# Kernel optimization log

Measured on AMD Instinct MI355X. Metric: run time of the kernel, lower is better.

Reference implementation:

```python
import jax, jax.numpy as jnp
import numpy as np

EPS = 1e-8
THRESHOLD_FACTOR = 0.5


def setup_inputs() -> dict:
    key = jax.random.key(0)
    k1, k2, k3 = jax.random.split(key, 3)
    B, S, D_IN, D_OUT = 4, 4096, 2048, 2048
    x = jax.random.normal(k1, (B, S, D_IN), dtype=jnp.float32)
    # kaiming-uniform-like init for weight
    bound = 1.0 / np.sqrt(D_IN)
    weight = jax.random.uniform(k2, (D_OUT, D_IN), dtype=jnp.float32,
                                minval=-np.sqrt(3.0) * bound, maxval=np.sqrt(3.0) * bound)
    row_scale = jnp.ones((D_OUT, 1), dtype=jnp.float32)
    bias = jax.random.uniform(k3, (D_OUT,), dtype=jnp.float32, minval=-bound, maxval=bound)
    g = jnp.ones((D_IN,), dtype=jnp.float32)  # input RMSNorm affine weight
    return {"x": x, "weight": weight, "row_scale": row_scale, "bias": bias, "g": g}


def _rms_norm(v, axis):
    return v * jax.lax.rsqrt(jnp.mean(v * v, axis=axis, keepdims=True) + EPS)


def reference(x, weight, row_scale, bias, g):
    # input RMSNorm with affine scale
    xn = _rms_norm(x, -1) * g  # [B,S,Din]
    # row RMSNorm of weight
    w = _rms_norm(weight, 1)  # [Dout,Din]
    # abs-mean threshold ternary quantization
    abs_mean = jnp.mean(jnp.abs(w), axis=1, keepdims=True)  # [Dout,1]
    mask = (jnp.abs(w) > THRESHOLD_FACTOR * abs_mean).astype(w.dtype)
    w_q = jnp.sign(w) * mask  # ternary {-1,0,1}
    # scaled dequant: per-row abs_mean and learned row_scale
    w_eff = w_q * abs_mean * row_scale  # [Dout,Din]
    out = jnp.einsum('bsd,od->bso', xn, w_eff) + bias
    return out
```

## Files before the change

kernel.cpp:

```cpp
#include <hip/hip_runtime.h>
#include <stdint.h>

#define EPSF 1e-8f

using i32x4 = __attribute__((ext_vector_type(4))) int;

__device__ __forceinline__ float wave_sum(float v) {
#pragma unroll
  for (int off = 32; off > 0; off >>= 1) v += __shfl_down(v, off, 64);
  return v;
}
__device__ __forceinline__ float wave_max(float v) {
#pragma unroll
  for (int off = 32; off > 0; off >>= 1) v = fmaxf(v, __shfl_down(v, off, 64));
  return v;
}

__global__ __launch_bounds__(256) void wquant_kernel(
    const float* __restrict__ w, const float* __restrict__ row_scale,
    signed char* __restrict__ wq, float* __restrict__ scale, int K) {
  const int row = blockIdx.x;
  const int t = threadIdx.x;
  const float* wr = w + (size_t)row * K;
  float4 v0 = reinterpret_cast<const float4*>(wr)[2 * t];
  float4 v1 = reinterpret_cast<const float4*>(wr)[2 * t + 1];
  float f[8] = {v0.x, v0.y, v0.z, v0.w, v1.x, v1.y, v1.z, v1.w};
  float sa = 0.f, sq = 0.f;
#pragma unroll
  for (int i = 0; i < 8; ++i) { sa += fabsf(f[i]); sq += f[i] * f[i]; }
  sa = wave_sum(sa);
  sq = wave_sum(sq);
  __shared__ float smA[4], smQ[4];
  const int wid = t >> 6;
  if ((t & 63) == 0) { smA[wid] = sa; smQ[wid] = sq; }
  __syncthreads();
  const float sumabs = smA[0] + smA[1] + smA[2] + smA[3];
  const float sumsq  = smQ[0] + smQ[1] + smQ[2] + smQ[3];
  const float absmean = sumabs / (float)K;
  const float thr = 0.5f * absmean;
  union { signed char c[8]; uint2 u; } pk;
#pragma unroll
  for (int i = 0; i < 8; ++i)
    pk.c[i] = (fabsf(f[i]) > thr) ? (f[i] > 0.f ? (signed char)1 : (signed char)-1)
                                  : (signed char)0;
  reinterpret_cast<uint2*>(wq + (size_t)row * K)[t] = pk.u;
  if (t == 0)
    scale[row] = absmean * rsqrtf(sumsq / (float)K + EPSF) * row_scale[row];
}

__global__ __launch_bounds__(256) void xnorm_kernel(
    const float* __restrict__ x, const float* __restrict__ g,
    signed char* __restrict__ xq, float* __restrict__ sx, int K) {
  const int row = blockIdx.x;
  const int t = threadIdx.x;
  const float* xr = x + (size_t)row * K;
  float4 v0 = reinterpret_cast<const float4*>(xr)[2 * t];
  float4 v1 = reinterpret_cast<const float4*>(xr)[2 * t + 1];
  float f[8] = {v0.x, v0.y, v0.z, v0.w, v1.x, v1.y, v1.z, v1.w};
  float sq = 0.f;
#pragma unroll
  for (int i = 0; i < 8; ++i) sq += f[i] * f[i];
  sq = wave_sum(sq);
  __shared__ float smQ[4], smM[4];
  const int wid = t >> 6;
  if ((t & 63) == 0) smQ[wid] = sq;
  __syncthreads();
  const float sumsq = smQ[0] + smQ[1] + smQ[2] + smQ[3];
  const float rs = rsqrtf(sumsq / (float)K + EPSF);
  float4 g0 = reinterpret_cast<const float4*>(g)[2 * t];
  float4 g1 = reinterpret_cast<const float4*>(g)[2 * t + 1];
  float gg[8] = {g0.x, g0.y, g0.z, g0.w, g1.x, g1.y, g1.z, g1.w};
  float vv[8]; float am = 0.f;
#pragma unroll
  for (int i = 0; i < 8; ++i) {
    vv[i] = f[i] * rs * gg[i];
    am = fmaxf(am, fabsf(vv[i]));
  }
  am = wave_max(am);
  if ((t & 63) == 0) smM[wid] = am;
  __syncthreads();
  const float amax = fmaxf(fmaxf(smM[0], smM[1]), fmaxf(smM[2], smM[3]));
  const float inv = amax > 0.f ? 127.f / amax : 0.f;
  union { signed char c[8]; uint2 u; } pk;
#pragma unroll
  for (int i = 0; i < 8; ++i)
    pk.c[i] = (signed char)__float2int_rn(vv[i] * inv);
  reinterpret_cast<uint2*>(xq + (size_t)row * K)[t] = pk.u;
  if (t == 0) sx[row] = amax > 0.f ? amax / 127.f : 0.f;
}


#define BAR() do { __builtin_amdgcn_sched_barrier(0); \
                   asm volatile("" ::: "memory"); \
                   __builtin_amdgcn_s_barrier(); \
                   asm volatile("" ::: "memory"); \
                   __builtin_amdgcn_sched_barrier(0); } while (0)
#define VM(n) asm volatile("s_waitcnt vmcnt(" #n ")" ::: "memory")

__global__ __launch_bounds__(512, 2) void gemm_kernel(
    const signed char* __restrict__ A,
    const signed char* __restrict__ B,
    const float* __restrict__ scale, const float* __restrict__ bias,
    const float* __restrict__ sx,
    float* __restrict__ C, int M, int N, int K) {
  __shared__ signed char lds[2][2][2][16384];

  const int tid  = threadIdx.x;
  const int lane = tid & 63;
  const int wid  = tid >> 6;
  const int wm   = wid >> 2;
  const int wn   = wid & 3;
  const int fr   = lane & 15;
  const int kq   = lane >> 4;

  const int nwg = gridDim.x;
  const int cpx = nwg >> 3;
  const int swz = (blockIdx.x & 7) * cpx + (blockIdx.x >> 3);
  const int NBN = N >> 8;
  const int bn = swz % NBN;
  const int bm = swz / NBN;
  const int mBase = bm * 256, nBase = bn * 256;

  const size_t Kb = (size_t)K;

  const int sr = tid >> 3;
  const int gsrc = ((tid & 7) - sr - (sr >> 3)) & 7;
  const char* Abyte = (const char*)A + (size_t)(mBase + sr) * Kb + gsrc * 16;
  const char* Bbyte = (const char*)B +
      (size_t)(nBase + ((sr >> 5) * 64) + (sr & 31)) * Kb + gsrc * 16;

#define STAGE_A(bufi, h, t) do { \
    __builtin_amdgcn_global_load_lds( \
      (const __attribute__((address_space(1))) void*)(Abyte + (size_t)((h) * 64) * Kb + (size_t)(t) * 128), \
      (__attribute__((address_space(3))) void*)(&lds[bufi][0][h][tid * 16]), 16, 0, 0); \
    __builtin_amdgcn_global_load_lds( \
      (const __attribute__((address_space(1))) void*)(Abyte + (size_t)(128 + (h) * 64) * Kb + (size_t)(t) * 128), \
      (__attribute__((address_space(3))) void*)(&lds[bufi][0][h][8192 + tid * 16]), 16, 0, 0); \
  } while (0)

#define STAGE_B(bufi, h, t) do { \
    __builtin_amdgcn_global_load_lds( \
      (const __attribute__((address_space(1))) void*)(Bbyte + (size_t)((h) * 32) * Kb + (size_t)(t) * 128), \
      (__attribute__((address_space(3))) void*)(&lds[bufi][1][h][tid * 16]), 16, 0, 0); \
    __builtin_amdgcn_global_load_lds( \
      (const __attribute__((address_space(1))) void*)(Bbyte + (size_t)(128 + (h) * 32) * Kb + (size_t)(t) * 128), \
      (__attribute__((address_space(3))) void*)(&lds[bufi][1][h][8192 + tid * 16]), 16, 0, 0); \
  } while (0)

  const int raBase = wm * 64 + fr;
  const int rbBase = wn * 32 + fr;
  const int pA = (raBase + (raBase >> 3)) & 7;
  const int pB = (rbBase + (rbBase >> 3)) & 7;

  i32x4 aF[4][2], bF[4][2];
  i32x4 acc[8][4];
#pragma unroll
  for (int m = 0; m < 8; ++m)
#pragma unroll
    for (int n = 0; n < 4; ++n) acc[m][n] = (i32x4){0, 0, 0, 0};

#define LDA(bufi, mg) do { \
    _Pragma("unroll") for (int mm = 0; mm < 4; ++mm) \
    _Pragma("unroll") for (int s = 0; s < 2; ++s) \
      aF[mm][s] = *(const i32x4*)&lds[bufi][0][mg][ \
          (raBase + mm * 16) * 128 + (((s * 4 + kq) + pA + 2 * mm) & 7) * 16]; \
  } while (0)

#define LDB(bufi, np) do { \
    _Pragma("unroll") for (int nn = 0; nn < 2; ++nn) \
    _Pragma("unroll") for (int s = 0; s < 2; ++s) \
      bF[(np) * 2 + nn][s] = *(const i32x4*)&lds[bufi][1][np][ \
          (rbBase + nn * 16) * 128 + (((s * 4 + kq) + pB + 2 * nn) & 7) * 16]; \
  } while (0)

#define MFMA_Q(mg, np) do { \
    __builtin_amdgcn_s_setprio(1); \
    _Pragma("unroll") for (int mm = 0; mm < 4; ++mm) \
    _Pragma("unroll") for (int nn = 0; nn < 2; ++nn) { \
      i32x4 c = acc[(mg) * 4 + mm][(np) * 2 + nn]; \
      c = __builtin_amdgcn_mfma_i32_16x16x64_i8(aF[mm][0], bF[(np) * 2 + nn][0], c, 0, 0, 0); \
      c = __builtin_amdgcn_mfma_i32_16x16x64_i8(aF[mm][1], bF[(np) * 2 + nn][1], c, 0, 0, 0); \
      acc[(mg) * 4 + mm][(np) * 2 + nn] = c; \
    } \
    __builtin_amdgcn_s_setprio(0); } while (0)

  const int crowBase = mBase + wm * 128 + kq * 4;
  const int ccolBase = nBase + wn * 64 + fr;

#define STORE_Q(mg, np) do { \
    float sxq_[4][4]; \
    _Pragma("unroll") for (int mm = 0; mm < 4; ++mm) \
    _Pragma("unroll") for (int r = 0; r < 4; ++r) \
      sxq_[mm][r] = sx[crowBase + ((mg) * 4 + mm) * 16 + r]; \
    _Pragma("unroll") for (int nn = 0; nn < 2; ++nn) { \
      const int gc = ccolBase + ((np) * 2 + nn) * 16; \
      const float sc = scale[gc]; \
      const float bi = bias[gc]; \
      _Pragma("unroll") for (int mm = 0; mm < 4; ++mm) { \
        const int r0 = crowBase + ((mg) * 4 + mm) * 16; \
        _Pragma("unroll") for (int r = 0; r < 4; ++r) \
          C[(size_t)(r0 + r) * (size_t)N + (size_t)gc] = \
              (float)acc[(mg) * 4 + mm][(np) * 2 + nn][r] * (sxq_[mm][r] * sc) + bi; \
      } } } while (0)

  STAGE_A(0, 0, 0); STAGE_B(0, 0, 0);
  STAGE_A(0, 1, 0); STAGE_B(0, 1, 0);
  STAGE_A(1, 0, 1); STAGE_B(1, 0, 1);
  VM(8);
  BAR();

  const int NT = K >> 7;
  for (int i = 0; i < (NT >> 1) - 1; ++i) {
    const int t1  = 2 * i + 1;
    const int tn0 = 2 * i + 2;
    const int tn1 = 2 * i + 3;
    LDA(0, 0); LDB(0, 0); STAGE_A(1, 1, t1); VM(6);
    BAR(); MFMA_Q(0, 0); BAR();
    LDB(0, 1); STAGE_B(1, 1, t1);
    BAR(); MFMA_Q(0, 1); BAR();
    LDA(0, 1); STAGE_A(0, 0, tn0);
    BAR(); MFMA_Q(1, 0); BAR();
    STAGE_B(0, 0, tn0); VM(8);
    BAR(); MFMA_Q(1, 1); BAR();
    LDA(1, 0); LDB(1, 0); STAGE_A(0, 1, tn0); VM(6);
    BAR(); MFMA_Q(0, 0); BAR();
    LDB(1, 1); STAGE_B(0, 1, tn0);
    BAR(); MFMA_Q(0, 1); BAR();
    LDA(1, 1); STAGE_A(1, 0, tn1);
    BAR(); MFMA_Q(1, 0); BAR();
    STAGE_B(1, 0, tn1); VM(8);
    BAR(); MFMA_Q(1, 1); BAR();
  }

  {
    const int tl = NT - 1;
    LDA(0, 0); LDB(0, 0); STAGE_A(1, 1, tl); VM(6);
    BAR(); MFMA_Q(0, 0); BAR();
    LDB(0, 1); STAGE_B(1, 1, tl);
    BAR(); MFMA_Q(0, 1); BAR();
    LDA(0, 1);
    BAR(); MFMA_Q(1, 0); BAR();
    VM(4);
    BAR(); MFMA_Q(1, 1); BAR();
    LDA(1, 0); LDB(1, 0); VM(0);
    BAR(); MFMA_Q(0, 0); STORE_Q(0, 0); BAR();
    LDB(1, 1);
    BAR(); MFMA_Q(0, 1); STORE_Q(0, 1); BAR();
    LDA(1, 1);
    BAR(); MFMA_Q(1, 0); STORE_Q(1, 0); BAR();
    MFMA_Q(1, 1); STORE_Q(1, 1);
  }
#undef STAGE_A
#undef STAGE_B
#undef LDA
#undef LDB
#undef MFMA_Q
#undef STORE_Q
}

extern "C" void kernel_launch(void* const* d_in, const int* in_sizes, int n_in,
                              void* d_out, int out_size, void* d_ws, size_t ws_size,
                              hipStream_t stream) {
  const float* x         = (const float*)d_in[0];
  const float* weight    = (const float*)d_in[1];
  const float* row_scale = (const float*)d_in[2];
  const float* bias      = (const float*)d_in[3];
  const float* g         = (const float*)d_in[4];
  float* out = (float*)d_out;

  const int Din  = in_sizes[4];
  const int Dout = in_sizes[3];
  const int Mrows = in_sizes[0] / Din;

  char* ws = (char*)d_ws;
  signed char* wq = (signed char*)ws;
  signed char* xq = (signed char*)(ws + (size_t)Dout * Din);
  float* scale = (float*)(ws + (size_t)Dout * Din + (size_t)Mrows * Din);
  float* sx = scale + Dout;

  wquant_kernel<<<Dout, 256, 0, stream>>>(weight, row_scale, wq, scale, Din);
  xnorm_kernel<<<Mrows, 256, 0, stream>>>(x, g, xq, sx, Din);
  const int grid = (Mrows / 256) * (Dout / 256);
  gemm_kernel<<<grid, 512, 0, stream>>>(xq, wq, scale, bias, sx, out,
                                        Mrows, Dout, Din);
}
```

Measured before the change: 124.4 us.

## Use XOR LDS swizzle and halve barriers in int8 MFMA GEMM main loop

```diff
diff --git a/kernel.cpp b/kernel.cpp
--- a/kernel.cpp
+++ b/kernel.cpp
@@ -124,7 +124,7 @@
   const size_t Kb = (size_t)K;
 
   const int sr = tid >> 3;
-  const int gsrc = ((tid & 7) - sr - (sr >> 3)) & 7;
+  const int gsrc = (tid & 7) ^ (sr & 7);
   const char* Abyte = (const char*)A + (size_t)(mBase + sr) * Kb + gsrc * 16;
   const char* Bbyte = (const char*)B +
       (size_t)(nBase + ((sr >> 5) * 64) + (sr & 31)) * Kb + gsrc * 16;
@@ -147,10 +147,9 @@
       (__attribute__((address_space(3))) void*)(&lds[bufi][1][h][8192 + tid * 16]), 16, 0, 0); \
   } while (0)
 
-  const int raBase = wm * 64 + fr;
-  const int rbBase = wn * 32 + fr;
-  const int pA = (raBase + (raBase >> 3)) & 7;
-  const int pB = (rbBase + (rbBase >> 3)) & 7;
+  const int slot0 = ((kq ^ (fr & 7)) << 4);
+  const int aRowB = (wm * 64 + fr) * 128;
+  const int bRowB = (wn * 32 + fr) * 128;
 
   i32x4 aF[4][2], bF[4][2];
   i32x4 acc[8][4];
@@ -163,14 +162,14 @@
     _Pragma("unroll") for (int mm = 0; mm < 4; ++mm) \
     _Pragma("unroll") for (int s = 0; s < 2; ++s) \
       aF[mm][s] = *(const i32x4*)&lds[bufi][0][mg][ \
-          (raBase + mm * 16) * 128 + (((s * 4 + kq) + pA + 2 * mm) & 7) * 16]; \
+          aRowB + mm * 2048 + (slot0 ^ (s << 6))]; \
   } while (0)
 
 #define LDB(bufi, np) do { \
     _Pragma("unroll") for (int nn = 0; nn < 2; ++nn) \
     _Pragma("unroll") for (int s = 0; s < 2; ++s) \
       bF[(np) * 2 + nn][s] = *(const i32x4*)&lds[bufi][1][np][ \
-          (rbBase + nn * 16) * 128 + (((s * 4 + kq) + pB + 2 * nn) & 7) * 16]; \
+          bRowB + nn * 2048 + (slot0 ^ (s << 6))]; \
   } while (0)
 
 #define MFMA_Q(mg, np) do { \
@@ -215,40 +214,40 @@
     const int tn0 = 2 * i + 2;
     const int tn1 = 2 * i + 3;
     LDA(0, 0); LDB(0, 0); STAGE_A(1, 1, t1); VM(6);
-    BAR(); MFMA_Q(0, 0); BAR();
+    BAR(); MFMA_Q(0, 0);
     LDB(0, 1); STAGE_B(1, 1, t1);
-    BAR(); MFMA_Q(0, 1); BAR();
+    BAR(); MFMA_Q(0, 1);
     LDA(0, 1); STAGE_A(0, 0, tn0);
-    BAR(); MFMA_Q(1, 0); BAR();
+    BAR(); MFMA_Q(1, 0);
     STAGE_B(0, 0, tn0); VM(8);
-    BAR(); MFMA_Q(1, 1); BAR();
+    BAR(); MFMA_Q(1, 1);
     LDA(1, 0); LDB(1, 0); STAGE_A(0, 1, tn0); VM(6);
-    BAR(); MFMA_Q(0, 0); BAR();
+    BAR(); MFMA_Q(0, 0);
     LDB(1, 1); STAGE_B(0, 1, tn0);
-    BAR(); MFMA_Q(0, 1); BAR();
+    BAR(); MFMA_Q(0, 1);
     LDA(1, 1); STAGE_A(1, 0, tn1);
-    BAR(); MFMA_Q(1, 0); BAR();
+    BAR(); MFMA_Q(1, 0);
     STAGE_B(1, 0, tn1); VM(8);
-    BAR(); MFMA_Q(1, 1); BAR();
+    BAR(); MFMA_Q(1, 1);
   }
 
   {
     const int tl = NT - 1;
     LDA(0, 0); LDB(0, 0); STAGE_A(1, 1, tl); VM(6);
-    BAR(); MFMA_Q(0, 0); BAR();
+    BAR(); MFMA_Q(0, 0);
     LDB(0, 1); STAGE_B(1, 1, tl);
-    BAR(); MFMA_Q(0, 1); BAR();
+    BAR(); MFMA_Q(0, 1);
     LDA(0, 1);
-    BAR(); MFMA_Q(1, 0); BAR();
+    BAR(); MFMA_Q(1, 0);
     VM(4);
-    BAR(); MFMA_Q(1, 1); BAR();
+    BAR(); MFMA_Q(1, 1);
     LDA(1, 0); LDB(1, 0); VM(0);
-    BAR(); MFMA_Q(0, 0); STORE_Q(0, 0); BAR();
+    BAR(); MFMA_Q(0, 0); STORE_Q(0, 0);
     LDB(1, 1);
-    BAR(); MFMA_Q(0, 1); STORE_Q(0, 1); BAR();
+    BAR(); MFMA_Q(0, 1); STORE_Q(0, 1);
     LDA(1, 1);
-    BAR(); MFMA_Q(1, 0); STORE_Q(1, 0); BAR();
-    MFMA_Q(1, 1); STORE_Q(1, 1);
+    BAR(); MFMA_Q(1, 0); STORE_Q(1, 0);
+    BAR(); MFMA_Q(1, 1); STORE_Q(1, 1);
   }
 #undef STAGE_A
 #undef STAGE_B
```

After: 114.2 us. 1.09x faster.
